# Kernel optimization log

Hardware: AMD Instinct MI355X
Metric: run time of the kernel (lower is better)

## Reference

```python
import jax, jax.numpy as jnp
import numpy as np


def _cell(h, c, x, Wih, Whh, b):
    # PyTorch LSTM cell: gates ordered [i, f, g, o], W_* shaped [4h, in]/[4h, h]
    gates = x @ Wih.T + h @ Whh.T + b  # [batch, 4h]
    i, f, g, o = jnp.split(gates, 4, axis=-1)
    c = jax.nn.sigmoid(f) * c + jax.nn.sigmoid(i) * jnp.tanh(g)
    h = jax.nn.sigmoid(o) * jnp.tanh(c)
    return h, c


def setup_inputs() -> dict:
    key = jax.random.key(0)
    ks = jax.random.split(key, 9)
    seq_len, batch, pose_dim, h_dim = 16, 32768, 34, 64
    s = 1.0 / np.sqrt(h_dim)  # PyTorch LSTM/Linear init range
    u = lambda k, shape: jax.random.uniform(k, shape, jnp.float32, -s, s)
    return {
        "obs_s": jax.random.normal(ks[0], (seq_len, batch, pose_dim), jnp.float32),
        "Wih_enc": u(ks[1], (4 * h_dim, pose_dim)),
        "Whh_enc": u(ks[2], (4 * h_dim, h_dim)),
        "b_enc": u(ks[3], (4 * h_dim,)),  # b_ih + b_hh fused
        "Wih_dec": u(ks[4], (4 * h_dim, pose_dim)),
        "Whh_dec": u(ks[5], (4 * h_dim, h_dim)),
        "b_dec": u(ks[6], (4 * h_dim,)),
        "fc_w": u(ks[7], (pose_dim, h_dim)),
        "fc_b": u(ks[8], (pose_dim,)),
        "pred_len": 15,
    }


def reference(obs_s, Wih_enc, Whh_enc, b_enc, Wih_dec, Whh_dec, b_dec, fc_w, fc_b, pred_len):
    batch = obs_s.shape[1]
    h_dim = Whh_enc.shape[1]
    h0 = jnp.zeros((batch, h_dim), obs_s.dtype)
    c0 = jnp.zeros((batch, h_dim), obs_s.dtype)

    def enc_step(carry, x):
        h, c = carry
        h, c = _cell(h, c, x, Wih_enc, Whh_enc, b_enc)
        return (h, c), None

    (h, c), _ = jax.lax.scan(enc_step, (h0, c0), obs_s)

    def dec_step(carry, _):
        h, c, last = carry
        h, c = _cell(h, c, last, Wih_dec, Whh_dec, b_dec)
        curr = h @ fc_w.T + fc_b  # [batch, pose_dim]
        # original feeds back curr_s.detach()
        return (h, c, jax.lax.stop_gradient(curr)), curr

    _, pred_s = jax.lax.scan(dec_step, (h, c, obs_s[-1]), None, length=pred_len)
    return pred_s  # [pred_len, batch, pose_dim]
```

## Files before the change

kernel.cpp:

```cpp
#include <hip/hip_runtime.h>

typedef _Float16 f16;
typedef _Float16 f16x8 __attribute__((ext_vector_type(8)));
typedef float f32x4 __attribute__((ext_vector_type(4)));

#define MFMA16(a, b, c) __builtin_amdgcn_mfma_f32_16x16x32_f16((a), (b), (c), 0, 0, 0)

constexpr int SEQ   = 16;
constexpr int PLEN  = 15;
constexpr int BATCH = 32768;
constexpr int POSE  = 34;
constexpr int HD    = 64;
constexpr int GRPS  = 2;
constexpr int ROWS  = 32;
constexpr int BROWS = GRPS * ROWS;
constexpr int XROW  = 136;

constexpr float LOG2E  = 1.4426950408889634f;
constexpr float LOG2E2 = 2.8853900817779268f;

__device__ __forceinline__ float rcpf(float x)   { return __builtin_amdgcn_rcpf(x); }
__device__ __forceinline__ float exp2f_(float x) { return __builtin_amdgcn_exp2f(x); }

__global__ __launch_bounds__(256, 2)
void lstm6(const float* __restrict__ obs,
           const float* __restrict__ Wih_e, const float* __restrict__ Whh_e,
           const float* __restrict__ b_e,
           const float* __restrict__ Wih_d, const float* __restrict__ Whh_d,
           const float* __restrict__ b_d,
           const float* __restrict__ fc_w, const float* __restrict__ fc_b,
           float* __restrict__ out)
{
    __shared__ f16 bfr[2 * GRPS * ROWS * XROW];

    const int tid  = threadIdx.x;
    const int lane = tid & 63;
    const int q    = tid >> 6;
    const int l15  = lane & 15;
    const int l4   = lane >> 4;
    const int blkbase = blockIdx.x * BROWS;

    f16x8 Bw[4][4];
    auto loadB = [&](const float* __restrict__ Wih, const float* __restrict__ Whh,
                     const float* __restrict__ b) {
        #pragma unroll
        for (int gg = 0; gg < 4; ++gg) {
            const int r = (gg * 4 + q) * 16 + l15;
            const float sc = (gg == 2) ? LOG2E2 : LOG2E;
            #pragma unroll
            for (int kf = 0; kf < 2; ++kf) {
                const float* src = Whh + r * HD + kf * 32 + l4 * 8;
                #pragma unroll
                for (int j = 0; j < 8; ++j) Bw[gg][kf][j] = (f16)(src[j] * sc);
            }
            {
                const float* src = Wih + r * POSE + l4 * 8;
                #pragma unroll
                for (int j = 0; j < 8; ++j) Bw[gg][2][j] = (f16)(src[j] * sc);
            }
            #pragma unroll
            for (int j = 0; j < 8; ++j) {
                const int k = 96 + l4 * 8 + j;
                float v = 0.f;
                if (k < 98)       v = Wih[r * POSE + (k - 64)];
                else if (k == 98) v = b[r];
                Bw[gg][3][j] = (f16)(v * sc);
            }
        }
    };
    loadB(Wih_e, Whh_e, b_e);

    auto stage_x = [&](int ts, int dstbuf) {
        const float* src = obs + ((size_t)ts * BATCH + blkbase) * POSE;
        #pragma unroll
        for (int it = 0; it < 9; ++it) {
            int i = it * 256 + tid;
            if (i < BROWS * POSE) {
                int row = i / POSE, col = i - row * POSE;
                bfr[((dstbuf * GRPS + (row >> 5)) * ROWS + (row & 31)) * XROW + HD + col] = (f16)src[i];
            }
        }
    };

    const int  p    = q * 16 + l15;
    const bool fcok = (q < 3);
    f16x8 Bfc[2];
    #pragma unroll
    for (int kf = 0; kf < 2; ++kf)
        #pragma unroll
        for (int j = 0; j < 8; ++j)
            Bfc[kf][j] = (f16)((fcok && p < POSE) ? fc_w[p * HD + kf * 32 + l4 * 8 + j] : 0.f);
    const float fcb = (fcok && p < POSE) ? fc_b[p] : 0.f;

    for (int i = tid; i < 2 * GRPS * ROWS * XROW; i += 256) {
        int c = i % XROW;
        bfr[i] = (c == 98) ? (f16)1.0f : (f16)0.0f;
    }
    __syncthreads();
    stage_x(0, 0);
    __syncthreads();

    f32x4 cst[GRPS][2];
    #pragma unroll
    for (int g = 0; g < GRPS; ++g) { cst[g][0] = (f32x4)0.f; cst[g][1] = (f32x4)0.f; }

    auto ldA = [&](int grp, int srcbuf, f16x8 (&a)[2][4]) {
        #pragma unroll
        for (int mf = 0; mf < 2; ++mf)
            #pragma unroll
            for (int kf = 0; kf < 4; ++kf)
                a[mf][kf] = *(const f16x8*)&bfr[((srcbuf * GRPS + grp) * ROWS + mf * 16 + l15) * XROW + kf * 32 + l4 * 8];
    };
    auto gates = [&](const f16x8 (&a)[2][4], f32x4 (&acc)[2][4]) {
        #pragma unroll
        for (int mf = 0; mf < 2; ++mf)
            #pragma unroll
            for (int gg = 0; gg < 4; ++gg) acc[mf][gg] = (f32x4)0.f;
        #pragma unroll
        for (int kf = 0; kf < 4; ++kf)
            #pragma unroll
            for (int gg = 0; gg < 4; ++gg) {
                acc[0][gg] = MFMA16(a[0][kf], Bw[gg][kf], acc[0][gg]);
                acc[1][gg] = MFMA16(a[1][kf], Bw[gg][kf], acc[1][gg]);
            }
    };
    auto nonlin = [&](int grp, f32x4 (&acc)[2][4], int dstbuf) {
        #pragma unroll
        for (int mf = 0; mf < 2; ++mf) {
            #pragma unroll
            for (int r = 0; r < 4; ++r) {
                float si = rcpf(1.f + exp2f_(-acc[mf][0][r]));
                float sf = rcpf(1.f + exp2f_(-acc[mf][1][r]));
                float tg = 1.f - 2.f * rcpf(1.f + exp2f_(acc[mf][2][r]));
                float so = rcpf(1.f + exp2f_(-acc[mf][3][r]));
                float c  = sf * cst[grp][mf][r] + si * tg;
                float tc = 1.f - 2.f * rcpf(1.f + exp2f_(c * LOG2E2));
                cst[grp][mf][r] = c;
                bfr[((dstbuf * GRPS + grp) * ROWS + mf * 16 + l4 * 4 + r) * XROW + q * 16 + l15] = (f16)(so * tc);
            }
        }
    };
    auto fc_step = [&](int grp, int srcbuf, int t) {
        if (!fcok) return;
        f16x8 ah[2][2];
        #pragma unroll
        for (int mf = 0; mf < 2; ++mf)
            #pragma unroll
            for (int kf = 0; kf < 2; ++kf)
                ah[mf][kf] = *(const f16x8*)&bfr[((srcbuf * GRPS + grp) * ROWS + mf * 16 + l15) * XROW + kf * 32 + l4 * 8];
        f32x4 o0 = {fcb, fcb, fcb, fcb}, o1 = {fcb, fcb, fcb, fcb};
        #pragma unroll
        for (int kf = 0; kf < 2; ++kf) {
            o0 = MFMA16(ah[0][kf], Bfc[kf], o0);
            o1 = MFMA16(ah[1][kf], Bfc[kf], o1);
        }
        if (p < POSE) {
            float* ob = out + ((size_t)t * BATCH + blkbase + grp * ROWS) * POSE;
            #pragma unroll
            for (int r = 0; r < 4; ++r) {
                int r0 = l4 * 4 + r, r1 = 16 + l4 * 4 + r;
                ob[r0 * POSE + p] = o0[r];
                ob[r1 * POSE + p] = o1[r];
                bfr[((srcbuf * GRPS + grp) * ROWS + r0) * XROW + HD + p] = (f16)o0[r];
                bfr[((srcbuf * GRPS + grp) * ROWS + r1) * XROW + HD + p] = (f16)o1[r];
            }
        }
    };

    int cur = 0;

    #pragma unroll 1
    for (int s = 0; s < SEQ; ++s) {
        const int nxt = cur ^ 1;
        f16x8 aA[2][4], aB[2][4];
        f32x4 accA[2][4], accB[2][4];
        ldA(0, cur, aA);
        gates(aA, accA);
        ldA(1, cur, aB);
        gates(aB, accB);
        { int ts = s + 1 < 15 ? s + 1 : 15; stage_x(ts, nxt); }
        nonlin(0, accA, nxt);
        nonlin(1, accB, nxt);
        __syncthreads();
        cur = nxt;
    }

    loadB(Wih_d, Whh_d, b_d);
    #pragma unroll 1
    for (int t = 0; t < PLEN; ++t) {
        const int nxt = cur ^ 1;
        f16x8 aA[2][4], aB[2][4];
        f32x4 accA[2][4], accB[2][4];
        ldA(0, cur, aA);
        gates(aA, accA);
        ldA(1, cur, aB);
        gates(aB, accB);
        nonlin(0, accA, nxt);
        nonlin(1, accB, nxt);
        __syncthreads();
        fc_step(0, nxt, t);
        fc_step(1, nxt, t);
        __syncthreads();
        cur = nxt;
    }
}

extern "C" void kernel_launch(void* const* d_in, const int* in_sizes, int n_in,
                              void* d_out, int out_size, void* d_ws, size_t ws_size,
                              hipStream_t stream) {
    const float* obs   = (const float*)d_in[0];
    const float* Wih_e = (const float*)d_in[1];
    const float* Whh_e = (const float*)d_in[2];
    const float* b_e   = (const float*)d_in[3];
    const float* Wih_d = (const float*)d_in[4];
    const float* Whh_d = (const float*)d_in[5];
    const float* b_d   = (const float*)d_in[6];
    const float* fc_w  = (const float*)d_in[7];
    const float* fc_b  = (const float*)d_in[8];
    float* out = (float*)d_out;

    lstm6<<<dim3(BATCH / BROWS), dim3(256), 0, stream>>>(
        obs, Wih_e, Whh_e, b_e, Wih_d, Whh_d, b_d, fc_w, fc_b, out);
}
```

Measured before the change: 128.2 us.

## Fold decoder feedback FC into recurrent weights and interleave four 16-row groups

Decoder steps after the first fold the FC feedback into the recurrent weights, W_eff = Whh + Wih·fc_w, with a matching bias. Each gate matmul then uses K=64 instead of 128, the FC output no longer goes back through shared memory, and one barrier per decoder step is removed. Rows are regrouped into four 16-row groups so MFMA, nonlinearity and FC work of different groups can be interleaved for ILP. Each thread now computes the folded weights with scalar loops at runtime, which adds startup cost. The f16 rounding of the fused weights may change numerics slightly.

```diff
diff --git a/kernel.cpp b/kernel.cpp
--- a/kernel.cpp
+++ b/kernel.cpp
@@ -11,8 +11,8 @@
 constexpr int BATCH = 32768;
 constexpr int POSE  = 34;
 constexpr int HD    = 64;
-constexpr int GRPS  = 2;
-constexpr int ROWS  = 32;
+constexpr int GRPS  = 4;
+constexpr int ROWS  = 16;
 constexpr int BROWS = GRPS * ROWS;
 constexpr int XROW  = 136;
 
@@ -23,7 +23,7 @@
 __device__ __forceinline__ float exp2f_(float x) { return __builtin_amdgcn_exp2f(x); }
 
 __global__ __launch_bounds__(256, 2)
-void lstm6(const float* __restrict__ obs,
+void lstm7(const float* __restrict__ obs,
            const float* __restrict__ Wih_e, const float* __restrict__ Whh_e,
            const float* __restrict__ b_e,
            const float* __restrict__ Wih_d, const float* __restrict__ Whh_d,
@@ -41,6 +41,7 @@
     const int blkbase = blockIdx.x * BROWS;
 
     f16x8 Bw[4][4];
+    float be[4];
     auto loadB = [&](const float* __restrict__ Wih, const float* __restrict__ Whh,
                      const float* __restrict__ b) {
         #pragma unroll
@@ -68,7 +69,32 @@
             }
         }
     };
-    loadB(Wih_e, Whh_e, b_e);
+
+    auto loadBeff = [&]() {
+        #pragma unroll
+        for (int gg = 0; gg < 4; ++gg) {
+            const int r = (gg * 4 + q) * 16 + l15;
+            const float sc = (gg == 2) ? LOG2E2 : LOG2E;
+            #pragma unroll
+            for (int kf = 0; kf < 2; ++kf) {
+                float a8[8];
+                const float* wh = Whh_d + r * HD + kf * 32 + l4 * 8;
+                #pragma unroll
+                for (int j = 0; j < 8; ++j) a8[j] = wh[j];
+                for (int pp = 0; pp < POSE; ++pp) {
+                    const float wp = Wih_d[r * POSE + pp];
+                    const float* fw = fc_w + pp * HD + kf * 32 + l4 * 8;
+                    #pragma unroll
+                    for (int j = 0; j < 8; ++j) a8[j] += wp * fw[j];
+                }
+                #pragma unroll
+                for (int j = 0; j < 8; ++j) Bw[gg][kf][j] = (f16)(a8[j] * sc);
+            }
+            float bb = b_d[r];
+            for (int pp = 0; pp < POSE; ++pp) bb += Wih_d[r * POSE + pp] * fc_b[pp];
+            be[gg] = bb * sc;
+        }
+    };
 
     auto stage_x = [&](int ts, int dstbuf) {
         const float* src = obs + ((size_t)ts * BATCH + blkbase) * POSE;
@@ -77,7 +103,7 @@
             int i = it * 256 + tid;
             if (i < BROWS * POSE) {
                 int row = i / POSE, col = i - row * POSE;
-                bfr[((dstbuf * GRPS + (row >> 5)) * ROWS + (row & 31)) * XROW + HD + col] = (f16)src[i];
+                bfr[((dstbuf * GRPS + (row >> 4)) * ROWS + (row & 15)) * XROW + HD + col] = (f16)src[i];
             }
         }
     };
@@ -92,6 +118,8 @@
             Bfc[kf][j] = (f16)((fcok && p < POSE) ? fc_w[p * HD + kf * 32 + l4 * 8 + j] : 0.f);
     const float fcb = (fcok && p < POSE) ? fc_b[p] : 0.f;
 
+    loadB(Wih_e, Whh_e, b_e);
+
     for (int i = tid; i < 2 * GRPS * ROWS * XROW; i += 256) {
         int c = i % XROW;
         bfr[i] = (c == 98) ? (f16)1.0f : (f16)0.0f;
@@ -100,70 +128,56 @@
     stage_x(0, 0);
     __syncthreads();
 
-    f32x4 cst[GRPS][2];
+    f32x4 cst[GRPS];
     #pragma unroll
-    for (int g = 0; g < GRPS; ++g) { cst[g][0] = (f32x4)0.f; cst[g][1] = (f32x4)0.f; }
-
-    auto ldA = [&](int grp, int srcbuf, f16x8 (&a)[2][4]) {
-        #pragma unroll
-        for (int mf = 0; mf < 2; ++mf)
-            #pragma unroll
-            for (int kf = 0; kf < 4; ++kf)
-                a[mf][kf] = *(const f16x8*)&bfr[((srcbuf * GRPS + grp) * ROWS + mf * 16 + l15) * XROW + kf * 32 + l4 * 8];
-    };
-    auto gates = [&](const f16x8 (&a)[2][4], f32x4 (&acc)[2][4]) {
-        #pragma unroll
-        for (int mf = 0; mf < 2; ++mf)
-            #pragma unroll
-            for (int gg = 0; gg < 4; ++gg) acc[mf][gg] = (f32x4)0.f;
+    for (int c = 0; c < GRPS; ++c) cst[c] = (f32x4)0.f;
+
+    auto ldA = [&](int c, int sb, f16x8 (&a)[4], int nkf) {
+        for (int kf = 0; kf < nkf; ++kf)
+            a[kf] = *(const f16x8*)&bfr[((sb * GRPS + c) * ROWS + l15) * XROW + kf * 32 + l4 * 8];
+    };
+    auto g128 = [&](const f16x8 (&a)[4], f32x4 (&acc)[4]) {
+        #pragma unroll
+        for (int gg = 0; gg < 4; ++gg) acc[gg] = (f32x4)0.f;
         #pragma unroll
         for (int kf = 0; kf < 4; ++kf)
             #pragma unroll
-            for (int gg = 0; gg < 4; ++gg) {
-                acc[0][gg] = MFMA16(a[0][kf], Bw[gg][kf], acc[0][gg]);
-                acc[1][gg] = MFMA16(a[1][kf], Bw[gg][kf], acc[1][gg]);
-            }
-    };
-    auto nonlin = [&](int grp, f32x4 (&acc)[2][4], int dstbuf) {
-        #pragma unroll
-        for (int mf = 0; mf < 2; ++mf) {
-            #pragma unroll
-            for (int r = 0; r < 4; ++r) {
-                float si = rcpf(1.f + exp2f_(-acc[mf][0][r]));
-                float sf = rcpf(1.f + exp2f_(-acc[mf][1][r]));
-                float tg = 1.f - 2.f * rcpf(1.f + exp2f_(acc[mf][2][r]));
-                float so = rcpf(1.f + exp2f_(-acc[mf][3][r]));
-                float c  = sf * cst[grp][mf][r] + si * tg;
-                float tc = 1.f - 2.f * rcpf(1.f + exp2f_(c * LOG2E2));
-                cst[grp][mf][r] = c;
-                bfr[((dstbuf * GRPS + grp) * ROWS + mf * 16 + l4 * 4 + r) * XROW + q * 16 + l15] = (f16)(so * tc);
-            }
-        }
-    };
-    auto fc_step = [&](int grp, int srcbuf, int t) {
+            for (int gg = 0; gg < 4; ++gg) acc[gg] = MFMA16(a[kf], Bw[gg][kf], acc[gg]);
+    };
+    auto g64 = [&](const f16x8 (&a)[4], f32x4 (&acc)[4]) {
+        #pragma unroll
+        for (int gg = 0; gg < 4; ++gg) acc[gg] = (f32x4){be[gg], be[gg], be[gg], be[gg]};
+        #pragma unroll
+        for (int kf = 0; kf < 2; ++kf)
+            #pragma unroll
+            for (int gg = 0; gg < 4; ++gg) acc[gg] = MFMA16(a[kf], Bw[gg][kf], acc[gg]);
+    };
+    auto nonlin = [&](int c, f32x4 (&acc)[4], int db) {
+        #pragma unroll
+        for (int r = 0; r < 4; ++r) {
+            float si = rcpf(1.f + exp2f_(-acc[0][r]));
+            float sf = rcpf(1.f + exp2f_(-acc[1][r]));
+            float tg = 1.f - 2.f * rcpf(1.f + exp2f_(acc[2][r]));
+            float so = rcpf(1.f + exp2f_(-acc[3][r]));
+            float cc = sf * cst[c][r] + si * tg;
+            float tc = 1.f - 2.f * rcpf(1.f + exp2f_(cc * LOG2E2));
+            cst[c][r] = cc;
+            bfr[((db * GRPS + c) * ROWS + l4 * 4 + r) * XROW + q * 16 + l15] = (f16)(so * tc);
+        }
+    };
+    auto fcst = [&](int c, int sb, int t) {
         if (!fcok) return;
-        f16x8 ah[2][2];
-        #pragma unroll
-        for (int mf = 0; mf < 2; ++mf)
-            #pragma unroll
-            for (int kf = 0; kf < 2; ++kf)
-                ah[mf][kf] = *(const f16x8*)&bfr[((srcbuf * GRPS + grp) * ROWS + mf * 16 + l15) * XROW + kf * 32 + l4 * 8];
-        f32x4 o0 = {fcb, fcb, fcb, fcb}, o1 = {fcb, fcb, fcb, fcb};
-        #pragma unroll
-        for (int kf = 0; kf < 2; ++kf) {
-            o0 = MFMA16(ah[0][kf], Bfc[kf], o0);
-            o1 = MFMA16(ah[1][kf], Bfc[kf], o1);
-        }
+        f16x8 ah[2];
+        #pragma unroll
+        for (int kf = 0; kf < 2; ++kf)
+            ah[kf] = *(const f16x8*)&bfr[((sb * GRPS + c) * ROWS + l15) * XROW + kf * 32 + l4 * 8];
+        f32x4 o = {fcb, fcb, fcb, fcb};
+        o = MFMA16(ah[0], Bfc[0], o);
+        o = MFMA16(ah[1], Bfc[1], o);
         if (p < POSE) {
-            float* ob = out + ((size_t)t * BATCH + blkbase + grp * ROWS) * POSE;
-            #pragma unroll
-            for (int r = 0; r < 4; ++r) {
-                int r0 = l4 * 4 + r, r1 = 16 + l4 * 4 + r;
-                ob[r0 * POSE + p] = o0[r];
-                ob[r1 * POSE + p] = o1[r];
-                bfr[((srcbuf * GRPS + grp) * ROWS + r0) * XROW + HD + p] = (f16)o0[r];
-                bfr[((srcbuf * GRPS + grp) * ROWS + r1) * XROW + HD + p] = (f16)o1[r];
-            }
+            float* ob = out + ((size_t)t * BATCH + blkbase + c * ROWS) * POSE;
+            #pragma unroll
+            for (int r = 0; r < 4; ++r) ob[(l4 * 4 + r) * POSE + p] = o[r];
         }
     };
 
@@ -172,37 +186,64 @@
     #pragma unroll 1
     for (int s = 0; s < SEQ; ++s) {
         const int nxt = cur ^ 1;
-        f16x8 aA[2][4], aB[2][4];
-        f32x4 accA[2][4], accB[2][4];
-        ldA(0, cur, aA);
-        gates(aA, accA);
-        ldA(1, cur, aB);
-        gates(aB, accB);
+        f16x8 a[GRPS][4];
+        f32x4 acc[GRPS][4];
+        ldA(0, cur, a[0], 4); g128(a[0], acc[0]);
+        ldA(1, cur, a[1], 4); g128(a[1], acc[1]);
+        nonlin(0, acc[0], nxt);
+        ldA(2, cur, a[2], 4); g128(a[2], acc[2]);
+        nonlin(1, acc[1], nxt);
+        ldA(3, cur, a[3], 4); g128(a[3], acc[3]);
         { int ts = s + 1 < 15 ? s + 1 : 15; stage_x(ts, nxt); }
-        nonlin(0, accA, nxt);
-        nonlin(1, accB, nxt);
+        nonlin(2, acc[2], nxt);
+        nonlin(3, acc[3], nxt);
         __syncthreads();
         cur = nxt;
     }
 
     loadB(Wih_d, Whh_d, b_d);
-    #pragma unroll 1
-    for (int t = 0; t < PLEN; ++t) {
+    {
         const int nxt = cur ^ 1;
-        f16x8 aA[2][4], aB[2][4];
-        f32x4 accA[2][4], accB[2][4];
-        ldA(0, cur, aA);
-        gates(aA, accA);
-        ldA(1, cur, aB);
-        gates(aB, accB);
-        nonlin(0, accA, nxt);
-        nonlin(1, accB, nxt);
-        __syncthreads();
-        fc_step(0, nxt, t);
-        fc_step(1, nxt, t);
+        f16x8 a[GRPS][4];
+        f32x4 acc[GRPS][4];
+        ldA(0, cur, a[0], 4); g128(a[0], acc[0]);
+        ldA(1, cur, a[1], 4); g128(a[1], acc[1]);
+        nonlin(0, acc[0], nxt);
+        ldA(2, cur, a[2], 4); g128(a[2], acc[2]);
+        nonlin(1, acc[1], nxt);
+        ldA(3, cur, a[3], 4); g128(a[3], acc[3]);
+        nonlin(2, acc[2], nxt);
+        nonlin(3, acc[3], nxt);
         __syncthreads();
         cur = nxt;
     }
+
+    loadBeff();
+
+    #pragma unroll 1
+    for (int t = 1; t < PLEN; ++t) {
+        const int nxt = cur ^ 1;
+        f16x8 a[GRPS][4];
+        f32x4 acc[GRPS][4];
+        ldA(0, cur, a[0], 2); g64(a[0], acc[0]);
+        ldA(1, cur, a[1], 2); g64(a[1], acc[1]);
+        fcst(0, cur, t - 1);
+        nonlin(0, acc[0], nxt);
+        ldA(2, cur, a[2], 2); g64(a[2], acc[2]);
+        fcst(1, cur, t - 1);
+        nonlin(1, acc[1], nxt);
+        ldA(3, cur, a[3], 2); g64(a[3], acc[3]);
+        fcst(2, cur, t - 1);
+        nonlin(2, acc[2], nxt);
+        fcst(3, cur, t - 1);
+        nonlin(3, acc[3], nxt);
+        __syncthreads();
+        cur = nxt;
+    }
+    fcst(0, cur, PLEN - 1);
+    fcst(1, cur, PLEN - 1);
+    fcst(2, cur, PLEN - 1);
+    fcst(3, cur, PLEN - 1);
 }
 
 extern "C" void kernel_launch(void* const* d_in, const int* in_sizes, int n_in,
@@ -219,6 +260,6 @@
     const float* fc_b  = (const float*)d_in[8];
     float* out = (float*)d_out;
 
-    lstm6<<<dim3(BATCH / BROWS), dim3(256), 0, stream>>>(
+    lstm7<<<dim3(BATCH / BROWS), dim3(256), 0, stream>>>(
         obs, Wih_e, Whh_e, b_e, Wih_d, Whh_d, b_d, fc_w, fc_b, out);
 }
```

After: 162.1 us. 26.4% more time.
